# Performance work log

Hardware: AMD Instinct MI355X
Metric: run time of the kernel (lower is better)

## Reference

```python
import jax, jax.numpy as jnp
import numpy as np

N_NODES = 100000
N_EDGES = 3200000


def setup_inputs() -> dict:
    key = jax.random.key(0)
    k1, k2, k3, k4 = jax.random.split(key, 4)
    x = jax.random.normal(k1, (N_NODES, 128), dtype=jnp.float32)
    edge_index = jax.random.randint(k2, (2, N_EDGES), 0, N_NODES, dtype=jnp.int64)
    W1 = jax.random.normal(k3, (128, 16), dtype=jnp.float32) * 0.1
    b1 = jnp.zeros((16,), dtype=jnp.float32)
    W2 = jax.random.normal(k4, (16, 1), dtype=jnp.float32) * 0.1
    b2 = jnp.zeros((1,), dtype=jnp.float32)
    return {"x": x, "edge_index": edge_index, "W1": W1, "b1": b1, "W2": W2, "b2": b2}


def _gcn_conv(h, row, col, norm, b, n):
    # message = h[src] * norm, scatter-add into dst (PyG source_to_target flow)
    msg = h[row] * norm[:, None]
    out = jax.ops.segment_sum(msg, col, num_segments=n)
    return out + b


def reference(x, edge_index, W1, b1, W2, b2):
    n = x.shape[0]
    loops = jnp.arange(n, dtype=edge_index.dtype)
    # GCN adds self-loops with weight 1
    row = jnp.concatenate([edge_index[0], loops])
    col = jnp.concatenate([edge_index[1], loops])
    ew = jnp.ones(row.shape[0], dtype=x.dtype)
    deg = jax.ops.segment_sum(ew, col, num_segments=n)
    dinv = jnp.where(deg > 0, deg ** -0.5, 0.0).astype(x.dtype)
    norm = dinv[row] * dinv[col]

    h = _gcn_conv(x @ W1, row, col, norm, b1, n)  # [N,16]
    h = jax.nn.relu(h)
    # dropout p=0.2 is identity in eval mode
    h = _gcn_conv(h @ W2, row, col, norm, b2, n)  # [N,1]
    return jax.nn.sigmoid(h).squeeze(-1)  # [N]
```

## Files before the change

### kernel.cpp

```cpp
#include <hip/hip_runtime.h>
#include <hip/hip_fp16.h>
#include <cstdint>


#define F_IN 128
#define F_HID 16
#define PB 1024
#define PT 8192
#define NBMAX 512
#define CAPMAX 15104

__global__ __launch_bounds__(PB) void partition_kernel(
    const int* __restrict__ row, const int* __restrict__ col,
    int* __restrict__ cursor,
    int* __restrict__ ping,
    int capB, int NB, int n_edges) {
    __shared__ int sh_hist[NBMAX];
    __shared__ int sh_scan[NBMAX];
    __shared__ int sh_cur[NBMAX];
    __shared__ int sh_base[NBMAX];
    __shared__ int sh_wsum[16];
    __shared__ int sh_packed[PT];
    __shared__ unsigned short sh_bkt[PT];

    int t = threadIdx.x;
    int lane = t & 63;
    int wv = t >> 6;
    int ntiles = (n_edges + PT - 1) / PT;
    bool vec_ok = ((n_edges & 3) == 0);

    for (int tile = blockIdx.x; tile < ntiles; tile += gridDim.x) {
        int tbase = tile * PT;
        int tcnt = min(PT, n_edges - tbase);

        if (t < NBMAX) sh_hist[t] = 0;
        __syncthreads();

        int e0 = tbase + t * 8;
        int pk[8], bb[8];
        if (vec_ok && e0 + 8 <= n_edges) {
            int4 a0 = *(const int4*)(row + e0);
            int4 a1 = *(const int4*)(row + e0 + 4);
            int4 c0 = *(const int4*)(col + e0);
            int4 c1 = *(const int4*)(col + e0 + 4);
            int rr[8] = {a0.x, a0.y, a0.z, a0.w, a1.x, a1.y, a1.z, a1.w};
            int cc[8] = {c0.x, c0.y, c0.z, c0.w, c1.x, c1.y, c1.z, c1.w};
#pragma unroll
            for (int k = 0; k < 8; k++) {
                bb[k] = cc[k] >> 8;
                pk[k] = rr[k] | ((cc[k] & 255) << 17);
                atomicAdd(&sh_hist[bb[k]], 1);
            }
        } else {
#pragma unroll
            for (int k = 0; k < 8; k++) {
                int e = e0 + k;
                bb[k] = -1;
                if (e < n_edges) {
                    int r = row[e];
                    int c = col[e];
                    bb[k] = c >> 8;
                    pk[k] = r | ((c & 255) << 17);
                    atomicAdd(&sh_hist[bb[k]], 1);
                }
            }
        }
        __syncthreads();

        {
            int v = (t < NBMAX) ? sh_hist[t] : 0;
            int incl = v;
#pragma unroll
            for (int off = 1; off < 64; off <<= 1) {
                int u = __shfl_up(incl, off, 64);
                if (lane >= off) incl += u;
            }
            if (lane == 63) sh_wsum[wv] = incl;
            __syncthreads();
            if (t < 16) {
                int s = sh_wsum[t];
#pragma unroll
                for (int off = 1; off < 16; off <<= 1) {
                    int u = __shfl_up(s, off, 16);
                    if (t >= off) s += u;
                }
                sh_wsum[t] = s;
            }
            __syncthreads();
            int wexcl = (wv > 0) ? sh_wsum[wv - 1] : 0;
            if (t < NBMAX) sh_scan[t] = incl + wexcl;
        }
        __syncthreads();

        if (t < NBMAX) {
            int h = sh_hist[t];
            sh_cur[t] = sh_scan[t] - h;
            sh_base[t] = (h > 0 && t < NB) ? atomicAdd(&cursor[t], h) : 0;
        }
        __syncthreads();

#pragma unroll
        for (int k = 0; k < 8; k++) {
            if (bb[k] >= 0) {
                int p = atomicAdd(&sh_cur[bb[k]], 1);
                sh_packed[p] = pk[k];
                sh_bkt[p] = (unsigned short)bb[k];
            }
        }
        __syncthreads();

#pragma unroll
        for (int k = 0; k < 8; k++) {
            int p = t + k * PB;
            if (p < tcnt) {
                int b = sh_bkt[p];
                int off = p - (sh_scan[b] - sh_hist[b]);
                int gp = sh_base[b] + off;
                if (gp < capB) ping[(size_t)b * capB + gp] = sh_packed[p];
            }
        }
        __syncthreads();
    }
}

__global__ __launch_bounds__(PB) void degree_kernel(
    const int* __restrict__ cursor, const int* __restrict__ ping,
    int* __restrict__ cnt, int* __restrict__ rowptr, int capB, int n) {
    __shared__ int hist[256];
    __shared__ int wsum[16];

    int b = blockIdx.x, t = threadIdx.x;
    int lane = t & 63;
    int wv = t >> 6;

    if (t < 256) hist[t] = 0;
    __syncthreads();

    int cb = min(cursor[b], capB);
    const int* src = ping + (size_t)b * capB;
    for (int i = t; i < cb; i += PB) {
        atomicAdd(&hist[(src[i] >> 17) & 255], 1);
    }
    __syncthreads();

    int incl = 0;
    {
        int v = (t < 256) ? hist[t] : 0;
        incl = v;
#pragma unroll
        for (int off = 1; off < 64; off <<= 1) {
            int u = __shfl_up(incl, off, 64);
            if (lane >= off) incl += u;
        }
        if (lane == 63) wsum[wv] = incl;
        __syncthreads();
        if (t < 16) {
            int s = wsum[t];
#pragma unroll
            for (int off = 1; off < 16; off <<= 1) {
                int u = __shfl_up(s, off, 16);
                if (t >= off) s += u;
            }
            wsum[t] = s;
        }
        __syncthreads();
    }

    if (t < 256) {
        int wexcl = (wv > 0) ? wsum[wv - 1] : 0;
        int h = hist[t];
        int excl = incl + wexcl - h;
        int g = b * 256 + t;
        if (g < n) {
            cnt[g] = h;
            rowptr[g] = b * capB + excl;
        }
    }
}

__global__ __launch_bounds__(256) void gemm1_kernel(const float* __restrict__ x,
                                                    const float* __restrict__ W1,
                                                    const int* __restrict__ cnt,
                                                    __half* __restrict__ h1p, int n) {
    __shared__ float sW[F_IN * F_HID];
    int tid = threadIdx.x;
    for (int i = tid; i < F_IN * F_HID; i += 256) sW[i] = W1[i];
    __syncthreads();

    int node = blockIdx.x * 256 + tid;
    if (node >= n) return;

    const float4* xr = (const float4*)(x + (size_t)node * F_IN);
    float acc[F_HID];
#pragma unroll
    for (int j = 0; j < F_HID; j++) acc[j] = 0.0f;

#pragma unroll 4
    for (int k4 = 0; k4 < F_IN / 4; k4++) {
        float4 xv = xr[k4];
        const float* w0 = &sW[(k4 * 4 + 0) * F_HID];
        const float* w1 = &sW[(k4 * 4 + 1) * F_HID];
        const float* w2 = &sW[(k4 * 4 + 2) * F_HID];
        const float* w3 = &sW[(k4 * 4 + 3) * F_HID];
#pragma unroll
        for (int j = 0; j < F_HID; j++) {
            acc[j] += xv.x * w0[j] + xv.y * w1[j] + xv.z * w2[j] + xv.w * w3[j];
        }
    }

    float d = rsqrtf((float)cnt[node] + 1.0f);
    __half2 hv[8];
#pragma unroll
    for (int j = 0; j < 8; j++) {
        hv[j] = __floats2half2_rn(acc[2 * j] * d, acc[2 * j + 1] * d);
    }
    float4* o4 = (float4*)(h1p + (size_t)node * F_HID);
    o4[0] = *(float4*)&hv[0];
    o4[1] = *(float4*)&hv[4];
}

__global__ __launch_bounds__(PB) void sort_gather1(
    const int* __restrict__ cursor, const int* __restrict__ ping,
    const int* __restrict__ cnt, const int* __restrict__ rowptr,
    const __half* __restrict__ h1p, const float* __restrict__ b1,
    const float* __restrict__ W2, float* __restrict__ sp,
    int* __restrict__ pong, int capB, int n) {
    extern __shared__ int B[];
    __shared__ int s_excl[256];
    __shared__ int s_h[256];
    __shared__ int cur[256];

    int b = blockIdx.x, t = threadIdx.x;

    if (t < 256) {
        int g = b * 256 + t;
        int h = (g < n) ? cnt[g] : 0;
        int excl = (g < n) ? (rowptr[g] - b * capB) : 0;
        s_h[t] = h;
        s_excl[t] = excl;
        cur[t] = excl;
    }
    __syncthreads();

    int cb = min(cursor[b], capB);
    const int* src = ping + (size_t)b * capB;

    for (int i = t; i < cb; i += PB) {
        int v = src[i];
        int p = atomicAdd(&cur[(v >> 17) & 255], 1);
        B[p] = v & 131071;
    }
    __syncthreads();

    for (int i = t; i < cb; i += PB) {
        pong[(size_t)b * capB + i] = B[i];
    }

    int l = t & 7;
    for (int j = t >> 3; j < 256; j += (PB >> 3)) {
        int g = b * 256 + j;
        if (g >= n) continue;
        int h = s_h[j];
        int base = s_excl[j];
        int end = base + h;

        float ax = 0.0f, ay = 0.0f;
        for (; base + 8 <= end; base += 8) {
#pragma unroll
            for (int m = 0; m < 8; m++) {
                int rm = B[base + m];
                float2 f = __half22float2(*(const __half2*)(h1p + (size_t)rm * F_HID + 2 * l));
                ax += f.x; ay += f.y;
            }
        }
        for (int m = 0; m < end - base; m++) {
            int rm = B[base + m];
            float2 f = __half22float2(*(const __half2*)(h1p + (size_t)rm * F_HID + 2 * l));
            ax += f.x; ay += f.y;
        }

        float dc = rsqrtf((float)h + 1.0f);
        float2 fs = __half22float2(*(const __half2*)(h1p + (size_t)g * F_HID + 2 * l));
        float v0 = (ax + fs.x) * dc + b1[2 * l];
        float v1 = (ay + fs.y) * dc + b1[2 * l + 1];
        v0 = fmaxf(v0, 0.0f);
        v1 = fmaxf(v1, 0.0f);
        float tt = v0 * W2[2 * l] + v1 * W2[2 * l + 1];
        tt += __shfl_xor(tt, 1, 8);
        tt += __shfl_xor(tt, 2, 8);
        tt += __shfl_xor(tt, 4, 8);
        if (l == 0) sp[g] = tt * dc;
    }
}

__global__ __launch_bounds__(256) void gather2_kernel(const int* __restrict__ rowptr,
                                                      const int* __restrict__ cnt,
                                                      const int* __restrict__ eidx,
                                                      const float* __restrict__ sp,
                                                      const float* __restrict__ b2,
                                                      float* __restrict__ out, int n) {
    int g = (blockIdx.x * 256 + threadIdx.x) >> 4;
    int lane = threadIdx.x & 15;
    if (g >= n) return;
    int start = rowptr[g];
    int end = start + cnt[g];

    float acc = 0.0f;
    for (int e = start + lane; e < end; e += 16) {
        acc += sp[eidx[e]];
    }
    acc += __shfl_xor(acc, 1, 16);
    acc += __shfl_xor(acc, 2, 16);
    acc += __shfl_xor(acc, 4, 16);
    acc += __shfl_xor(acc, 8, 16);
    if (lane == 0) {
        float v = (acc + sp[g]) * rsqrtf((float)cnt[g] + 1.0f) + b2[0];
        out[g] = 1.0f / (1.0f + __expf(-v));
    }
}

__global__ void bucket_scatter_kernel(const int* __restrict__ row,
                                      const int* __restrict__ col,
                                      int* __restrict__ cnt,
                                      int* __restrict__ eidx,
                                      int cap, int n_edges) {
    int e = blockIdx.x * blockDim.x + threadIdx.x;
    if (e < n_edges) {
        int c = col[e];
        int p = atomicAdd(&cnt[c], 1);
        if (p < cap) eidx[(size_t)c * cap + p] = row[e];
    }
}

__global__ __launch_bounds__(256) void gemm1f_kernel(const float* __restrict__ x,
                                                     const float* __restrict__ W1,
                                                     const int* __restrict__ cnt,
                                                     float* __restrict__ h1p, int n) {
    __shared__ float sW[F_IN * F_HID];
    int tid = threadIdx.x;
    for (int i = tid; i < F_IN * F_HID; i += 256) sW[i] = W1[i];
    __syncthreads();
    int node = blockIdx.x * 256 + tid;
    if (node >= n) return;
    const float4* xr = (const float4*)(x + (size_t)node * F_IN);
    float acc[F_HID];
#pragma unroll
    for (int j = 0; j < F_HID; j++) acc[j] = 0.0f;
#pragma unroll 4
    for (int k4 = 0; k4 < F_IN / 4; k4++) {
        float4 xv = xr[k4];
        const float* w0 = &sW[(k4 * 4 + 0) * F_HID];
        const float* w1 = &sW[(k4 * 4 + 1) * F_HID];
        const float* w2 = &sW[(k4 * 4 + 2) * F_HID];
        const float* w3 = &sW[(k4 * 4 + 3) * F_HID];
#pragma unroll
        for (int j = 0; j < F_HID; j++) {
            acc[j] += xv.x * w0[j] + xv.y * w1[j] + xv.z * w2[j] + xv.w * w3[j];
        }
    }
    float d = rsqrtf((float)cnt[node] + 1.0f);
    float4* outp = (float4*)(h1p + (size_t)node * F_HID);
    outp[0] = make_float4(acc[0] * d, acc[1] * d, acc[2] * d, acc[3] * d);
    outp[1] = make_float4(acc[4] * d, acc[5] * d, acc[6] * d, acc[7] * d);
    outp[2] = make_float4(acc[8] * d, acc[9] * d, acc[10] * d, acc[11] * d);
    outp[3] = make_float4(acc[12] * d, acc[13] * d, acc[14] * d, acc[15] * d);
}

__global__ __launch_bounds__(256) void fb_gather1_kernel(const int* __restrict__ cnt,
                                                         const int* __restrict__ eidx,
                                                         const float* __restrict__ h1p,
                                                         const float* __restrict__ b1,
                                                         const float* __restrict__ W2,
                                                         float* __restrict__ sp,
                                                         int cap, int n) {
    int g = (blockIdx.x * 256 + threadIdx.x) >> 4;
    int lane = threadIdx.x & 15;
    if (g >= n) return;
    int start = g * cap;
    int end = start + min(cnt[g], cap);
    float acc = 0.0f;
    for (int base = start; base < end; base += 16) {
        int e = base + lane;
        int r = (e < end) ? eidx[e] : 0;
        int m_cnt = min(16, end - base);
        for (int m = 0; m < m_cnt; m++) {
            int rm = __shfl(r, m, 16);
            acc += h1p[(size_t)rm * F_HID + lane];
        }
    }
    float dc = rsqrtf((float)cnt[g] + 1.0f);
    float v = (acc + h1p[(size_t)g * F_HID + lane]) * dc + b1[lane];
    v = fmaxf(v, 0.0f);
    float t = v * W2[lane];
    t += __shfl_xor(t, 1, 16);
    t += __shfl_xor(t, 2, 16);
    t += __shfl_xor(t, 4, 16);
    t += __shfl_xor(t, 8, 16);
    if (lane == 0) sp[g] = t * dc;
}

__global__ __launch_bounds__(256) void fb_gather2_kernel(const int* __restrict__ cnt,
                                                         const int* __restrict__ eidx,
                                                         const float* __restrict__ sp,
                                                         const float* __restrict__ b2,
                                                         float* __restrict__ out,
                                                         int cap, int n) {
    int g = (blockIdx.x * 256 + threadIdx.x) >> 4;
    int lane = threadIdx.x & 15;
    if (g >= n) return;
    int start = g * cap;
    int end = start + min(cnt[g], cap);
    float acc = 0.0f;
    for (int e = start + lane; e < end; e += 16) {
        acc += sp[eidx[e]];
    }
    acc += __shfl_xor(acc, 1, 16);
    acc += __shfl_xor(acc, 2, 16);
    acc += __shfl_xor(acc, 4, 16);
    acc += __shfl_xor(acc, 8, 16);
    if (lane == 0) {
        float v = (acc + sp[g]) * rsqrtf((float)cnt[g] + 1.0f) + b2[0];
        out[g] = 1.0f / (1.0f + __expf(-v));
    }
}

extern "C" void kernel_launch(void* const* d_in, const int* in_sizes, int n_in,
                              void* d_out, int out_size, void* d_ws, size_t ws_size,
                              hipStream_t stream) {
    const float* x  = (const float*)d_in[0];
    const int*   ei = (const int*)d_in[1];
    const float* W1 = (const float*)d_in[2];
    const float* b1 = (const float*)d_in[3];
    const float* W2 = (const float*)d_in[4];
    const float* b2 = (const float*)d_in[5];
    float* out = (float*)d_out;

    const int n = in_sizes[0] / F_IN;
    const int n_edges = in_sizes[1] / 2;
    const int* row = ei;
    const int* col = ei + n_edges;

    const size_t S = ((size_t)n + 511) & ~(size_t)511;
    const size_t words = ws_size / 4;

    const int B = 256;
    const int gridE = (n_edges + B - 1) / B;
    const int gridN = (n + B - 1) / B;

    const int NB = (n + 255) >> 8;
    int meanB = (NB > 0) ? (n_edges / NB) : 0;
    int capB = ((meanB + meanB / 8 + 1024) + 15) & ~15;
    size_t need_new = 11 * S + (size_t)NBMAX + 2 * (size_t)NB * (size_t)capB;

    if (n <= 131072 && NB <= NBMAX && capB <= CAPMAX && words >= need_new) {
        int*    cnt    = (int*)d_ws;
        int*    cursor = cnt + S;
        int*    rowptr = cursor + NBMAX;
        float*  sp     = (float*)(rowptr + S);
        __half* h1p    = (__half*)(sp + S);
        int*    ping   = (int*)(sp + S) + 8 * S;
        int*    pong   = ping + (size_t)NB * capB;

        hipMemsetAsync(cursor, 0, NBMAX * sizeof(int), stream);
        int ntiles = (n_edges + PT - 1) / PT;
        int pgrid = min(2048, ntiles);
        partition_kernel<<<pgrid, PB, 0, stream>>>(row, col, cursor, ping,
                                                   capB, NB, n_edges);
        degree_kernel<<<NB, PB, 0, stream>>>(cursor, ping, cnt, rowptr, capB, n);
        gemm1_kernel<<<gridN, B, 0, stream>>>(x, W1, cnt, h1p, n);
        sort_gather1<<<NB, PB, (size_t)capB * sizeof(int), stream>>>(
            cursor, ping, cnt, rowptr, h1p, b1, W2, sp, pong, capB, n);
        int gridG2 = (n * 16 + B - 1) / B;
        gather2_kernel<<<gridG2, B, 0, stream>>>(rowptr, cnt, pong, sp, b2, out, n);
    } else {
        int*   cnt  = (int*)d_ws;
        float* sp   = (float*)(cnt + S);
        float* h1pf = sp + S;
        int*   eidx = (int*)(h1pf + 16 * S);
        size_t tail_words = (words > 18 * S) ? (words - 18 * S) : 0;
        int cap = (int)min((size_t)96, tail_words / (size_t)(n > 0 ? n : 1));
        const int gridG = (n * 16 + B - 1) / B;

        hipMemsetAsync(cnt, 0, (size_t)n * sizeof(int), stream);
        bucket_scatter_kernel<<<gridE, B, 0, stream>>>(row, col, cnt, eidx, cap, n_edges);
        gemm1f_kernel<<<gridN, B, 0, stream>>>(x, W1, cnt, h1pf, n);
        fb_gather1_kernel<<<gridG, B, 0, stream>>>(cnt, eidx, h1pf, b1, W2, sp, cap, n);
        fb_gather2_kernel<<<gridG, B, 0, stream>>>(cnt, eidx, sp, b2, out, cap, n);
    }
}
```

Before: 182.1 us.

## Fuse degree histogram into GEMM1 kernel and halve partition tile size

Merges the per-bucket degree histogram/scan kernel with the x@W1 GEMM kernel, so each 256-thread block computes the degrees of its 256 nodes and then immediately does their projection, using the degree held in a register instead of re-reading cnt. This removes one launch and a global round-trip for cnt. It also halves the partition tile (4 edges per thread instead of 8), which gives more tiles and blocks for the partition pass but more global cursor atomics per edge. The histogram loop now runs with 256 threads instead of 1024, so per-bucket counting is less parallel.

```diff
diff --git a/kernel.cpp b/kernel.cpp
--- a/kernel.cpp
+++ b/kernel.cpp
@@ -6,7 +6,8 @@
 #define F_IN 128
 #define F_HID 16
 #define PB 1024
-#define PT 8192
+#define PT 4096
+#define EPT (PT / PB)
 #define NBMAX 512
 #define CAPMAX 15104
 
@@ -36,24 +37,22 @@
         if (t < NBMAX) sh_hist[t] = 0;
         __syncthreads();
 
-        int e0 = tbase + t * 8;
-        int pk[8], bb[8];
-        if (vec_ok && e0 + 8 <= n_edges) {
+        int e0 = tbase + t * EPT;
+        int pk[EPT], bb[EPT];
+        if (vec_ok && e0 + EPT <= n_edges) {
             int4 a0 = *(const int4*)(row + e0);
-            int4 a1 = *(const int4*)(row + e0 + 4);
             int4 c0 = *(const int4*)(col + e0);
-            int4 c1 = *(const int4*)(col + e0 + 4);
-            int rr[8] = {a0.x, a0.y, a0.z, a0.w, a1.x, a1.y, a1.z, a1.w};
-            int cc[8] = {c0.x, c0.y, c0.z, c0.w, c1.x, c1.y, c1.z, c1.w};
-#pragma unroll
-            for (int k = 0; k < 8; k++) {
+            int rr[EPT] = {a0.x, a0.y, a0.z, a0.w};
+            int cc[EPT] = {c0.x, c0.y, c0.z, c0.w};
+#pragma unroll
+            for (int k = 0; k < EPT; k++) {
                 bb[k] = cc[k] >> 8;
                 pk[k] = rr[k] | ((cc[k] & 255) << 17);
                 atomicAdd(&sh_hist[bb[k]], 1);
             }
         } else {
 #pragma unroll
-            for (int k = 0; k < 8; k++) {
+            for (int k = 0; k < EPT; k++) {
                 int e = e0 + k;
                 bb[k] = -1;
                 if (e < n_edges) {
@@ -100,7 +99,7 @@
         __syncthreads();
 
 #pragma unroll
-        for (int k = 0; k < 8; k++) {
+        for (int k = 0; k < EPT; k++) {
             if (bb[k] >= 0) {
                 int p = atomicAdd(&sh_cur[bb[k]], 1);
                 sh_packed[p] = pk[k];
@@ -110,7 +109,7 @@
         __syncthreads();
 
 #pragma unroll
-        for (int k = 0; k < 8; k++) {
+        for (int k = 0; k < EPT; k++) {
             int p = t + k * PB;
             if (p < tcnt) {
                 int b = sh_bkt[p];
@@ -123,72 +122,57 @@
     }
 }
 
-__global__ __launch_bounds__(PB) void degree_kernel(
+__global__ __launch_bounds__(256) void deg_gemm1_kernel(
     const int* __restrict__ cursor, const int* __restrict__ ping,
-    int* __restrict__ cnt, int* __restrict__ rowptr, int capB, int n) {
+    const float* __restrict__ x, const float* __restrict__ W1,
+    int* __restrict__ cnt, int* __restrict__ rowptr,
+    __half* __restrict__ h1p, int capB, int n) {
+    __shared__ float sW[F_IN * F_HID];
     __shared__ int hist[256];
-    __shared__ int wsum[16];
+    __shared__ int wsum[4];
 
     int b = blockIdx.x, t = threadIdx.x;
     int lane = t & 63;
     int wv = t >> 6;
 
-    if (t < 256) hist[t] = 0;
+    for (int i = t; i < F_IN * F_HID; i += 256) sW[i] = W1[i];
+    hist[t] = 0;
     __syncthreads();
 
     int cb = min(cursor[b], capB);
     const int* src = ping + (size_t)b * capB;
-    for (int i = t; i < cb; i += PB) {
+    for (int i = t; i < cb; i += 256) {
         atomicAdd(&hist[(src[i] >> 17) & 255], 1);
     }
     __syncthreads();
 
-    int incl = 0;
-    {
-        int v = (t < 256) ? hist[t] : 0;
-        incl = v;
-#pragma unroll
-        for (int off = 1; off < 64; off <<= 1) {
-            int u = __shfl_up(incl, off, 64);
-            if (lane >= off) incl += u;
-        }
-        if (lane == 63) wsum[wv] = incl;
-        __syncthreads();
-        if (t < 16) {
-            int s = wsum[t];
-#pragma unroll
-            for (int off = 1; off < 16; off <<= 1) {
-                int u = __shfl_up(s, off, 16);
-                if (t >= off) s += u;
-            }
-            wsum[t] = s;
-        }
-        __syncthreads();
-    }
-
-    if (t < 256) {
-        int wexcl = (wv > 0) ? wsum[wv - 1] : 0;
-        int h = hist[t];
-        int excl = incl + wexcl - h;
-        int g = b * 256 + t;
-        if (g < n) {
-            cnt[g] = h;
-            rowptr[g] = b * capB + excl;
-        }
-    }
-}
-
-__global__ __launch_bounds__(256) void gemm1_kernel(const float* __restrict__ x,
-                                                    const float* __restrict__ W1,
-                                                    const int* __restrict__ cnt,
-                                                    __half* __restrict__ h1p, int n) {
-    __shared__ float sW[F_IN * F_HID];
-    int tid = threadIdx.x;
-    for (int i = tid; i < F_IN * F_HID; i += 256) sW[i] = W1[i];
-    __syncthreads();
-
-    int node = blockIdx.x * 256 + tid;
+    int h = hist[t];
+    int incl = h;
+#pragma unroll
+    for (int off = 1; off < 64; off <<= 1) {
+        int u = __shfl_up(incl, off, 64);
+        if (lane >= off) incl += u;
+    }
+    if (lane == 63) wsum[wv] = incl;
+    __syncthreads();
+    if (t < 4) {
+        int s = wsum[t];
+#pragma unroll
+        for (int off = 1; off < 4; off <<= 1) {
+            int u = __shfl_up(s, off, 4);
+            if (t >= off) s += u;
+        }
+        wsum[t] = s;
+    }
+    __syncthreads();
+
+    int node = b * 256 + t;
     if (node >= n) return;
+
+    int wexcl = (wv > 0) ? wsum[wv - 1] : 0;
+    int excl = incl + wexcl - h;
+    cnt[node] = h;
+    rowptr[node] = b * capB + excl;
 
     const float4* xr = (const float4*)(x + (size_t)node * F_IN);
     float acc[F_HID];
@@ -208,7 +192,7 @@
         }
     }
 
-    float d = rsqrtf((float)cnt[node] + 1.0f);
+    float d = rsqrtf((float)h + 1.0f);
     __half2 hv[8];
 #pragma unroll
     for (int j = 0; j < 8; j++) {
@@ -466,8 +450,8 @@
         int pgrid = min(2048, ntiles);
         partition_kernel<<<pgrid, PB, 0, stream>>>(row, col, cursor, ping,
                                                    capB, NB, n_edges);
-        degree_kernel<<<NB, PB, 0, stream>>>(cursor, ping, cnt, rowptr, capB, n);
-        gemm1_kernel<<<gridN, B, 0, stream>>>(x, W1, cnt, h1p, n);
+        deg_gemm1_kernel<<<NB, B, 0, stream>>>(cursor, ping, x, W1, cnt,
+                                               rowptr, h1p, capB, n);
         sort_gather1<<<NB, PB, (size_t)capB * sizeof(int), stream>>>(
             cursor, ping, cnt, rowptr, h1p, b1, W2, sp, pong, capB, n);
         int gridG2 = (n * 16 + B - 1) / B;
```

Measured after the change: 189.3 us. 4.0% more time.
